# Kernel optimization log

Measured on AMD Instinct MI355X. Metric: run time of the kernel, lower is better.

The kernel has to match this reference:

```python
import jax, jax.numpy as jnp
import numpy as np

NUM_NODES = 8192
EMBED_DIM = 64
CURV = 1.0
EPS = 1e-08


def setup_inputs() -> dict:
    key = jax.random.key(0)
    emb = jax.random.normal(key, (NUM_NODES, EMBED_DIM), dtype=jnp.float32)
    return {"emb": emb}


def reference(emb):
    # emb: [N, D]
    norm_sq = jnp.sum(emb * emb, axis=-1, keepdims=True)            # [N, 1]
    dot = emb @ emb.T                                               # [N, N]
    # Pairwise squared distance via GEMM expansion (same math as the
    # explicit (e_i - e_j)^2 sum the original materializes as N x N x D).
    numerator = jnp.maximum(norm_sq + norm_sq.T - 2.0 * dot, 0.0)   # [N, N]
    # Faithful to the original: (1 - norm_i) * (1 - norm_j).T is [N,1]*[N,1]
    # -> a per-row column vector that broadcasts across columns.
    denominator = (1.0 - norm_sq) * (1.0 - norm_sq) + EPS           # [N, 1]
    dist = jnp.arccosh(1.0 + 2.0 * numerator / denominator + EPS)   # [N, N]
    adp = jnp.exp(-dist * CURV)
    adp = adp / (jnp.sum(adp, axis=1, keepdims=True) + EPS)
    return adp
```

## Files before the change

### kernel.cpp

```cpp
#include <hip/hip_runtime.h>
#include <hip/hip_bf16.h>
#include <stdint.h>
#include <type_traits>


#define N 8192
#define D 64
#define EPSF 1e-8f

typedef __bf16 bf16x8 __attribute__((ext_vector_type(8)));
typedef float  f32x4  __attribute__((ext_vector_type(4)));

static __device__ __forceinline__ unsigned short f32_to_bf16_rne(float f) {
    union { float f; uint32_t u; } c; c.f = f;
    return (unsigned short)((c.u + 0x7FFFu + ((c.u >> 16) & 1u)) >> 16);
}

__global__ __launch_bounds__(256) void prep_kernel(
    const float* __restrict__ emb, unsigned short* __restrict__ eh,
    float* __restrict__ nrm, float* __restrict__ rowsum)
{
    int tid = blockIdx.x * 256 + threadIdx.x;
    if (tid < N) rowsum[tid] = 0.0f;
    int row = tid >> 6;
    int k   = tid & 63;
    float v = emb[(size_t)row * D + k];
    eh[(size_t)row * D + k] = f32_to_bf16_rne(v);
    float sq = v * v;
    #pragma unroll
    for (int m = 32; m; m >>= 1) sq += __shfl_xor(sq, m, 64);
    if (k == 0) nrm[row] = sq;
}

template <bool STORE>
__global__ __launch_bounds__(256) void gemm_epi_kernel(
    const unsigned short* __restrict__ eh, const float* __restrict__ nrm,
    float* __restrict__ out, float* __restrict__ rowsum)
{
    const int lane = threadIdx.x & 63;
    const int wid  = threadIdx.x >> 6;
    const int bx = blockIdx.x & 63;
    const int by = blockIdx.x >> 6;
    const int brow = by * 128 + (wid >> 1) * 64;
    const int bcol = bx * 128 + (wid & 1) * 64;
    const int lr = lane & 15;
    const int lk = (lane >> 4) * 8;

    bf16x8 ah[4][2];
    #pragma unroll
    for (int g = 0; g < 4; ++g)
        #pragma unroll
        for (int h = 0; h < 2; ++h)
            ah[g][h] = *reinterpret_cast<const bf16x8*>(eh + (size_t)(brow + g*16 + lr) * D + h*32 + lk);

    float ni[4][4], rd2[4][4], sc[4][4];
    #pragma unroll
    for (int rg = 0; rg < 4; ++rg) {
        const int ibase = brow + rg * 16 + (lane >> 4) * 4;
        #pragma unroll
        for (int r = 0; r < 4; ++r) {
            ni[rg][r] = nrm[ibase + r];
            float om = 1.0f - ni[rg][r];
            rd2[rg][r] = 2.0f * __builtin_amdgcn_rcpf(om * om + EPSF);
            if (STORE) sc[rg][r] = __builtin_amdgcn_rcpf(rowsum[ibase + r] + EPSF);
        }
    }

    float rs[4][4];
    if (!STORE)
        #pragma unroll
        for (int rg = 0; rg < 4; ++rg)
            #pragma unroll
            for (int r = 0; r < 4; ++r) rs[rg][r] = 0.0f;

    auto body = [&](auto diag_c) {
        constexpr bool DIAG = decltype(diag_c)::value;
        #pragma unroll
        for (int cg = 0; cg < 4; ++cg) {
            bf16x8 bh[2];
            #pragma unroll
            for (int h = 0; h < 2; ++h)
                bh[h] = *reinterpret_cast<const bf16x8*>(eh + (size_t)(bcol + cg*16 + lr) * D + h*32 + lk);
            const int j = bcol + cg * 16 + lr;
            const float nj = nrm[j];
            #pragma unroll
            for (int rg = 0; rg < 4; ++rg) {
                f32x4 acc = (f32x4){0.f, 0.f, 0.f, 0.f};
                acc = __builtin_amdgcn_mfma_f32_16x16x32_bf16(ah[rg][0], bh[0], acc, 0, 0, 0);
                acc = __builtin_amdgcn_mfma_f32_16x16x32_bf16(ah[rg][1], bh[1], acc, 0, 0, 0);
                const int ibase = brow + rg * 16 + (lane >> 4) * 4;
                #pragma unroll
                for (int r = 0; r < 4; ++r) {
                    float num = fmaxf(fmaf(-2.0f, acc[r], ni[rg][r] + nj), 0.0f);
                    if (DIAG) { if (ibase + r == j) num = 0.0f; }
                    float t = fmaf(num, rd2[rg][r], EPSF);
                    float s = fmaf(t, t, t + t);
                    float adp = __builtin_amdgcn_rcpf((1.0f + t) + __builtin_amdgcn_sqrtf(s));
                    if (STORE) {
                        out[(size_t)(ibase + r) * N + j] = adp * sc[rg][r];
                    } else {
                        rs[rg][r] += adp;
                    }
                }
            }
        }
    };
    if (bx == by) body(std::true_type{});
    else          body(std::false_type{});

    if (!STORE) {
        #pragma unroll
        for (int rg = 0; rg < 4; ++rg) {
            const int ibase = brow + rg * 16 + (lane >> 4) * 4;
            #pragma unroll
            for (int r = 0; r < 4; ++r) {
                float v = rs[rg][r];
                v += __shfl_xor(v, 1, 64);
                v += __shfl_xor(v, 2, 64);
                v += __shfl_xor(v, 4, 64);
                v += __shfl_xor(v, 8, 64);
                if (lr == 0) atomicAdd(&rowsum[ibase + r], v);
            }
        }
    }
}

extern "C" void kernel_launch(void* const* d_in, const int* in_sizes, int n_in,
                              void* d_out, int out_size, void* d_ws, size_t ws_size,
                              hipStream_t stream)
{
    const float* emb = (const float*)d_in[0];
    float* out = (float*)d_out;
    char* ws = (char*)d_ws;
    unsigned short* eh = (unsigned short*)ws;
    float* nrm  = (float*)(ws + (size_t)N * D * 2);
    float* rsum = nrm + N;

    hipLaunchKernelGGL(prep_kernel, dim3((N * D) / 256), dim3(256), 0, stream,
                       emb, eh, nrm, rsum);
    hipLaunchKernelGGL((gemm_epi_kernel<false>), dim3((N/128)*(N/128)), dim3(256), 0, stream,
                       eh, nrm, out, rsum);
    hipLaunchKernelGGL((gemm_epi_kernel<true>),  dim3((N/128)*(N/128)), dim3(256), 0, stream,
                       eh, nrm, out, rsum);
}
```

Before: 355.1 us.

## Simplify epilogue math, use nontemporal stores, and aggregate row sums in LDS

Rewrites the distance-to-affinity epilogue so exp(-arccosh(x)) is computed as (1+t)-sqrt(t^2+2t), removing a reciprocal, and folds per-row constants into FMAs. Output writes use nontemporal stores to avoid cache pollution. Row-sum partials are first reduced in shared memory so each block issues one global atomic per row instead of one per wave. The subtraction form may lose precision when t is large.

```diff
diff --git a/kernel.cpp b/kernel.cpp
--- a/kernel.cpp
+++ b/kernel.cpp
@@ -46,6 +46,12 @@
     const int lr = lane & 15;
     const int lk = (lane >> 4) * 8;
 
+    __shared__ float lrs[128];
+    if (!STORE) {
+        if (threadIdx.x < 128) lrs[threadIdx.x] = 0.0f;
+        __syncthreads();
+    }
+
     bf16x8 ah[4][2];
     #pragma unroll
     for (int g = 0; g < 4; ++g)
@@ -53,16 +59,18 @@
         for (int h = 0; h < 2; ++h)
             ah[g][h] = *reinterpret_cast<const bf16x8*>(eh + (size_t)(brow + g*16 + lr) * D + h*32 + lk);
 
-    float ni[4][4], rd2[4][4], sc[4][4];
+    float rd2[4][4], ci[4][4], mi[4][4], sc[4][4];
     #pragma unroll
     for (int rg = 0; rg < 4; ++rg) {
         const int ibase = brow + rg * 16 + (lane >> 4) * 4;
         #pragma unroll
         for (int r = 0; r < 4; ++r) {
-            ni[rg][r] = nrm[ibase + r];
-            float om = 1.0f - ni[rg][r];
+            float ni = nrm[ibase + r];
+            float om = 1.0f - ni;
             rd2[rg][r] = 2.0f * __builtin_amdgcn_rcpf(om * om + EPSF);
+            ci[rg][r]  = fmaf(ni, rd2[rg][r], EPSF);
             if (STORE) sc[rg][r] = __builtin_amdgcn_rcpf(rowsum[ibase + r] + EPSF);
+            else       mi[rg][r] = -2.0f * rd2[rg][r];
         }
     }
 
@@ -91,13 +99,17 @@
                 const int ibase = brow + rg * 16 + (lane >> 4) * 4;
                 #pragma unroll
                 for (int r = 0; r < 4; ++r) {
-                    float num = fmaxf(fmaf(-2.0f, acc[r], ni[rg][r] + nj), 0.0f);
-                    if (DIAG) { if (ibase + r == j) num = 0.0f; }
-                    float t = fmaf(num, rd2[rg][r], EPSF);
-                    float s = fmaf(t, t, t + t);
-                    float adp = __builtin_amdgcn_rcpf((1.0f + t) + __builtin_amdgcn_sqrtf(s));
+                    float f1 = fmaf(nj, rd2[rg][r], ci[rg][r]);
+                    float t0;
+                    if (STORE) t0 = fmaf(-2.0f, acc[r] * rd2[rg][r], f1);
+                    else       t0 = fmaf(acc[r], mi[rg][r], f1);
+                    float t = fmaxf(t0, EPSF);
+                    if (DIAG) { if (ibase + r == j) t = EPSF; }
+                    float s = __builtin_amdgcn_sqrtf(fmaf(t, t, t + t));
+                    float adp = (1.0f + t) - s;
                     if (STORE) {
-                        out[(size_t)(ibase + r) * N + j] = adp * sc[rg][r];
+                        __builtin_nontemporal_store(adp * sc[rg][r],
+                            out + (size_t)(ibase + r) * N + j);
                     } else {
                         rs[rg][r] += adp;
                     }
@@ -111,7 +123,7 @@
     if (!STORE) {
         #pragma unroll
         for (int rg = 0; rg < 4; ++rg) {
-            const int ibase = brow + rg * 16 + (lane >> 4) * 4;
+            const int rowloc = (wid >> 1) * 64 + rg * 16 + (lane >> 4) * 4;
             #pragma unroll
             for (int r = 0; r < 4; ++r) {
                 float v = rs[rg][r];
@@ -119,9 +131,12 @@
                 v += __shfl_xor(v, 2, 64);
                 v += __shfl_xor(v, 4, 64);
                 v += __shfl_xor(v, 8, 64);
-                if (lr == 0) atomicAdd(&rowsum[ibase + r], v);
+                if (lr == 0) atomicAdd(&lrs[rowloc + r], v);
             }
         }
+        __syncthreads();
+        if (threadIdx.x < 128)
+            atomicAdd(&rowsum[by * 128 + threadIdx.x], lrs[threadIdx.x]);
     }
 }
 
```

New measurement: 348.3 us. About the same (-1.9%).
